# Kernel optimization log

Measured on AMD Instinct MI355X. Metric: run time of the kernel, lower is better.

Reference implementation:

```python
import jax, jax.numpy as jnp
import numpy as np

N = 100000      # nodes
E = 1600000     # edges (avg degree 16)
F_IN = 128      # node feature dim
F_E = 8         # edge feature dim
H = 4           # attention heads (layer 1)
C = 16          # hidden per head
T = 1           # target size (layer 2, heads=1, concat=False)
NEG_SLOPE = 0.2


def setup_inputs() -> dict:
    key = jax.random.key(0)
    ks = jax.random.split(key, 20)
    g = lambda k, shape, fan: (jax.random.normal(k, shape, jnp.float32) / np.sqrt(fan))
    return {
        "x": jax.random.normal(ks[0], (N, F_IN), jnp.float32),
        "edge_index": jax.random.randint(ks[1], (2, E), 0, N, dtype=jnp.int32),
        "edge_attr": jax.random.normal(ks[2], (E, F_E), jnp.float32),
        # layer 1 (in=F_IN, out=C, heads=H, concat=True, edge_dim=F_E)
        "Wl1": g(ks[3], (F_IN, H * C), F_IN),
        "bl1": jnp.zeros((H * C,), jnp.float32),
        "Wr1": g(ks[4], (F_IN, H * C), F_IN),
        "br1": jnp.zeros((H * C,), jnp.float32),
        "We1": g(ks[5], (F_E, H * C), F_E),
        "att1": g(ks[6], (H, C), C),
        "b1": jnp.zeros((H * C,), jnp.float32),
        # layer 2 (in=H*C, out=T, heads=1, concat=False, edge_dim=F_E)
        "Wl2": g(ks[7], (H * C, T), H * C),
        "bl2": jnp.zeros((T,), jnp.float32),
        "Wr2": g(ks[8], (H * C, T), H * C),
        "br2": jnp.zeros((T,), jnp.float32),
        "We2": g(ks[9], (F_E, T), F_E),
        "att2": g(ks[10], (1, T), T),
        "b2": jnp.zeros((T,), jnp.float32),
    }


def _gatv2(x, src, dst, eattr, Wl, bl, Wr, br, We, att, bias, heads, out_ch, concat, n_nodes):
    # add self loops, self-loop edge_attr = mean of edge_attr (PyG fill_value='mean')
    loop = jnp.arange(n_nodes, dtype=src.dtype)
    src_a = jnp.concatenate([src, loop])
    dst_a = jnp.concatenate([dst, loop])
    ea = jnp.concatenate(
        [eattr, jnp.broadcast_to(eattr.mean(axis=0), (n_nodes, eattr.shape[1]))], axis=0)

    xl = (x @ Wl + bl).reshape(n_nodes, heads, out_ch)   # source transform
    xr = (x @ Wr + br).reshape(n_nodes, heads, out_ch)   # target transform
    ee = (ea @ We).reshape(-1, heads, out_ch)            # edge transform (no bias)

    # GATv2: score = att . LeakyReLU(x_l[src] + x_r[dst] + W_e e)
    s = jax.nn.leaky_relu(xl[src_a] + xr[dst_a] + ee, NEG_SLOPE)  # [Ea,H,C]
    logits = jnp.einsum('ehc,hc->eh', s, att)                      # [Ea,H]

    # segment softmax over destination nodes (every node has a self loop)
    m = jax.ops.segment_max(logits, dst_a, num_segments=n_nodes)   # [N,H]
    p = jnp.exp(logits - m[dst_a])
    denom = jax.ops.segment_sum(p, dst_a, num_segments=n_nodes)
    alpha = p / denom[dst_a]                                        # [Ea,H]

    out = jax.ops.segment_sum(xl[src_a] * alpha[:, :, None], dst_a,
                              num_segments=n_nodes)                 # [N,H,C]
    out = out.reshape(n_nodes, heads * out_ch) if concat else out.mean(axis=1)
    return out + bias


def reference(x, edge_index, edge_attr, Wl1, bl1, Wr1, br1, We1, att1, b1,
              Wl2, bl2, Wr2, br2, We2, att2, b2):
    src, dst = edge_index[0], edge_index[1]
    # dropout layers are identity at eval time (training=False)
    h = _gatv2(x, src, dst, edge_attr, Wl1, bl1, Wr1, br1, We1, att1, b1,
               H, C, True, N)
    h = jax.nn.elu(h)
    out = _gatv2(h, src, dst, edge_attr, Wl2, bl2, Wr2, br2, We2, att2, b2,
                 1, T, False, N)
    return out
```

## Files before the change

kernel.cpp:

```cpp
#include <hip/hip_runtime.h>
#include <hip/hip_fp16.h>
#include <math.h>

#define N_NODES 100000
#define N_EDGES 1600000
#define N_ITEMS (N_EDGES + N_NODES)
#define F_IN 128
#define F_E 8
#define HC 64
#define NHEAD 4
#define NEG 0.2f
#define SCAN_BS 1024
#define SCAN_NB ((N_NODES + SCAN_BS - 1) / SCAN_BS)
#define MS_BLOCKS 1024
#define NEG_BIG (-3.0e38f)

union H2I { __half2 h; int i; };

__global__ void mean_sum_kernel(const float* __restrict__ ea, float* __restrict__ partials,
                                unsigned* __restrict__ deg) {
    __shared__ float sh[4][8];
    int stride = gridDim.x * blockDim.x;
    for (int i = blockIdx.x * blockDim.x + threadIdx.x; i < N_NODES; i += stride)
        deg[i] = 1u;
    float acc[8] = {0.f,0.f,0.f,0.f,0.f,0.f,0.f,0.f};
    for (int r = blockIdx.x * blockDim.x + threadIdx.x; r < N_EDGES; r += stride) {
        const float4* p = (const float4*)(ea + (size_t)r * 8);
        float4 a = p[0], b = p[1];
        acc[0] += a.x; acc[1] += a.y; acc[2] += a.z; acc[3] += a.w;
        acc[4] += b.x; acc[5] += b.y; acc[6] += b.z; acc[7] += b.w;
    }
    int wid  = threadIdx.x >> 6;
    int lane = threadIdx.x & 63;
#pragma unroll
    for (int k = 0; k < 8; k++) {
        float v = acc[k];
        for (int off = 32; off; off >>= 1) v += __shfl_down(v, off);
        if (lane == 0) sh[wid][k] = v;
    }
    __syncthreads();
    if (threadIdx.x < 8) {
        float s = sh[0][threadIdx.x] + sh[1][threadIdx.x] + sh[2][threadIdx.x] + sh[3][threadIdx.x];
        partials[blockIdx.x * 8 + threadIdx.x] = s;
    }
}

__global__ void reduce_sum8(const float* __restrict__ partials, float* __restrict__ sum8) {
    int lane = threadIdx.x;
    int c = lane & 7, g = lane >> 3;
    float s = 0.f;
    for (int b = g; b < MS_BLOCKS; b += 8) s += partials[b * 8 + c];
    s += __shfl_xor(s, 8);
    s += __shfl_xor(s, 16);
    s += __shfl_xor(s, 32);
    if (lane < 8) sum8[lane] = s;
}

__global__ void hist_kernel(const int* __restrict__ dst, unsigned* __restrict__ deg) {
    int e = blockIdx.x * blockDim.x + threadIdx.x;
    if (e < N_EDGES) atomicAdd(&deg[dst[e]], 1u);
}

__global__ void scan1(const unsigned* __restrict__ deg, unsigned* __restrict__ local_inc,
                      unsigned* __restrict__ bsum) {
    __shared__ unsigned tmp[SCAN_BS];
    int i = blockIdx.x * SCAN_BS + threadIdx.x;
    unsigned v = (i < N_NODES) ? deg[i] : 0u;
    tmp[threadIdx.x] = v;
    __syncthreads();
    for (int off = 1; off < SCAN_BS; off <<= 1) {
        unsigned add = (threadIdx.x >= (unsigned)off) ? tmp[threadIdx.x - off] : 0u;
        __syncthreads();
        tmp[threadIdx.x] += add;
        __syncthreads();
    }
    if (i < N_NODES) local_inc[i] = tmp[threadIdx.x];
    if (threadIdx.x == SCAN_BS - 1) bsum[blockIdx.x] = tmp[threadIdx.x];
}

__global__ void scan2(unsigned* __restrict__ bsum) {
    __shared__ unsigned tmp[128];
    int t = threadIdx.x;
    unsigned v = (t < SCAN_NB) ? bsum[t] : 0u;
    tmp[t] = v;
    __syncthreads();
    for (int off = 1; off < 128; off <<= 1) {
        unsigned add = (t >= off) ? tmp[t - off] : 0u;
        __syncthreads();
        tmp[t] += add;
        __syncthreads();
    }
    if (t < SCAN_NB) bsum[t] = tmp[t] - v;
}

__global__ void scan3(const unsigned* __restrict__ local_inc, const unsigned* __restrict__ deg,
                      const unsigned* __restrict__ bsum,
                      unsigned* __restrict__ row_start, unsigned* __restrict__ next) {
    int i = blockIdx.x * blockDim.x + threadIdx.x;
    if (i >= N_NODES) return;
    unsigned v = local_inc[i] - deg[i] + bsum[i / SCAN_BS];
    row_start[i] = v;
    next[i] = v;
}

__global__ void scatter_kernel(const int* __restrict__ src, const int* __restrict__ dst,
                               const float* __restrict__ ea, const float* __restrict__ sum8,
                               const float* __restrict__ We2,
                               unsigned* __restrict__ next,
                               int* __restrict__ sorted_src, __half* __restrict__ seah,
                               float* __restrict__ see2) {
    int item = blockIdx.x * blockDim.x + threadIdx.x;
    if (item >= N_ITEMS) return;
    int s, d;
    float4 a, b;
    if (item < N_EDGES) {
        s = src[item]; d = dst[item];
        const float4* p = (const float4*)(ea + (size_t)item * 8);
        a = p[0]; b = p[1];
    } else {
        s = d = item - N_EDGES;
        const float inv = 1.0f / N_EDGES;
        a = make_float4(sum8[0]*inv, sum8[1]*inv, sum8[2]*inv, sum8[3]*inv);
        b = make_float4(sum8[4]*inv, sum8[5]*inv, sum8[6]*inv, sum8[7]*inv);
    }
    float ee2 = a.x*We2[0] + a.y*We2[1] + a.z*We2[2] + a.w*We2[3]
              + b.x*We2[4] + b.y*We2[5] + b.z*We2[6] + b.w*We2[7];
    unsigned pos = atomicAdd(&next[d], 1u);
    sorted_src[pos] = s;
    see2[pos] = ee2;
    H2I p0, p1, p2, p3;
    p0.h = __floats2half2_rn(a.x, a.y);
    p1.h = __floats2half2_rn(a.z, a.w);
    p2.h = __floats2half2_rn(b.x, b.y);
    p3.h = __floats2half2_rn(b.z, b.w);
    *(int4*)(seah + (size_t)pos * 8) = make_int4(p0.i, p1.i, p2.i, p3.i);
}

__global__ __launch_bounds__(256) void gemm1_kernel(
        const float* __restrict__ x,
        const float* __restrict__ Wl, const float* __restrict__ bl,
        const float* __restrict__ Wr, const float* __restrict__ br,
        __half* __restrict__ xlh, float* __restrict__ xr) {
    __shared__ float xs_t[F_IN][36];
    int t = threadIdx.x & 31;
    int g = threadIdx.x >> 5;
    const float* Wsel = (t < 16) ? Wl : Wr;
    const float* bsel = (t < 16) ? bl : br;
    int jc = (t < 16) ? 4 * t : 4 * t - HC;
    float4 bias = *(const float4*)(bsel + jc);

    int n0 = blockIdx.x * 32;
    int row = threadIdx.x >> 3;
    int cq  = threadIdx.x & 7;
#pragma unroll
    for (int r = 0; r < 4; r++) {
        int c = cq * 4 + r * 32;
        float4 v = *(const float4*)(x + (size_t)(n0 + row) * F_IN + c);
        xs_t[c + 0][row] = v.x;
        xs_t[c + 1][row] = v.y;
        xs_t[c + 2][row] = v.z;
        xs_t[c + 3][row] = v.w;
    }
    __syncthreads();
    int nb = g * 4;
    float4 a0 = bias, a1 = bias, a2 = bias, a3 = bias;
#pragma unroll 4
    for (int k = 0; k < F_IN; k++) {
        float4 w  = *(const float4*)(Wsel + k * HC + jc);
        float4 xv = *(const float4*)&xs_t[k][nb];
        a0.x += w.x * xv.x; a0.y += w.y * xv.x; a0.z += w.z * xv.x; a0.w += w.w * xv.x;
        a1.x += w.x * xv.y; a1.y += w.y * xv.y; a1.z += w.z * xv.y; a1.w += w.w * xv.y;
        a2.x += w.x * xv.z; a2.y += w.y * xv.z; a2.z += w.z * xv.z; a2.w += w.w * xv.z;
        a3.x += w.x * xv.w; a3.y += w.y * xv.w; a3.z += w.z * xv.w; a3.w += w.w * xv.w;
    }
    if (t < 16) {
        float4 arr[4] = {a0, a1, a2, a3};
#pragma unroll
        for (int r = 0; r < 4; r++) {
            H2I u0, u1;
            u0.h = __floats2half2_rn(arr[r].x, arr[r].y);
            u1.h = __floats2half2_rn(arr[r].z, arr[r].w);
            *(int2*)(xlh + (size_t)(n0 + nb + r) * HC + jc) = make_int2(u0.i, u1.i);
        }
    } else {
        *(float4*)(xr + (size_t)(n0 + nb + 0) * HC + jc) = a0;
        *(float4*)(xr + (size_t)(n0 + nb + 1) * HC + jc) = a1;
        *(float4*)(xr + (size_t)(n0 + nb + 2) * HC + jc) = a2;
        *(float4*)(xr + (size_t)(n0 + nb + 3) * HC + jc) = a3;
    }
}

__device__ __forceinline__ void load_edge(const int* __restrict__ ssrc,
                                          const __half* __restrict__ seah,
                                          const __half* __restrict__ xlh,
                                          unsigned start, unsigned cnt, unsigned idx, int cl,
                                          bool& valid, float4& e0, float4& e1, float4& xv) {
    valid = (idx < cnt);
    unsigned sf = valid ? start + idx : start;
    int s = ssrc[sf];
    int4 r = *(const int4*)(seah + (size_t)sf * 8);
    H2I h0, h1, h2, h3;
    h0.i = r.x; h1.i = r.y; h2.i = r.z; h3.i = r.w;
    float2 f0 = __half22float2(h0.h), f1 = __half22float2(h1.h);
    float2 f2 = __half22float2(h2.h), f3 = __half22float2(h3.h);
    e0 = make_float4(f0.x, f0.y, f1.x, f1.y);
    e1 = make_float4(f2.x, f2.y, f3.x, f3.y);
    int2 xw = *(const int2*)(xlh + (size_t)s * HC + 4 * cl);
    H2I u0, u1; u0.i = xw.x; u1.i = xw.y;
    float2 g0 = __half22float2(u0.h), g1 = __half22float2(u1.h);
    xv = make_float4(g0.x, g0.y, g1.x, g1.y);
}

__device__ __forceinline__ void edge_update(const float4* __restrict__ we,
                                            const float4& attv, const float4& xrv,
                                            bool valid, const float4& ea0, const float4& ea1,
                                            const float4& xlv,
                                            float& m, float& den, float4& acc) {
    float4 v;
    v.x = xlv.x + xrv.x + ea0.x*we[0].x + ea0.y*we[1].x + ea0.z*we[2].x + ea0.w*we[3].x
                        + ea1.x*we[4].x + ea1.y*we[5].x + ea1.z*we[6].x + ea1.w*we[7].x;
    v.y = xlv.y + xrv.y + ea0.x*we[0].y + ea0.y*we[1].y + ea0.z*we[2].y + ea0.w*we[3].y
                        + ea1.x*we[4].y + ea1.y*we[5].y + ea1.z*we[6].y + ea1.w*we[7].y;
    v.z = xlv.z + xrv.z + ea0.x*we[0].z + ea0.y*we[1].z + ea0.z*we[2].z + ea0.w*we[3].z
                        + ea1.x*we[4].z + ea1.y*we[5].z + ea1.z*we[6].z + ea1.w*we[7].z;
    v.w = xlv.w + xrv.w + ea0.x*we[0].w + ea0.y*we[1].w + ea0.z*we[2].w + ea0.w*we[3].w
                        + ea1.x*we[4].w + ea1.y*we[5].w + ea1.z*we[6].w + ea1.w*we[7].w;
    v.x = v.x > 0.f ? v.x : NEG * v.x;
    v.y = v.y > 0.f ? v.y : NEG * v.y;
    v.z = v.z > 0.f ? v.z : NEG * v.z;
    v.w = v.w > 0.f ? v.w : NEG * v.w;
    float prod = v.x*attv.x + v.y*attv.y + v.z*attv.z + v.w*attv.w;
    prod += __shfl_xor(prod, 1);
    prod += __shfl_xor(prod, 2);
    float logit = valid ? prod : NEG_BIG;
    float mnew  = fmaxf(m, logit);
    float scale = __expf(m - mnew);
    float p     = valid ? __expf(logit - mnew) : 0.f;
    den   = den   * scale + p;
    acc.x = acc.x * scale + p * xlv.x;
    acc.y = acc.y * scale + p * xlv.y;
    acc.z = acc.z * scale + p * xlv.z;
    acc.w = acc.w * scale + p * xlv.w;
    m = mnew;
}

__global__ void gat1_kernel(const unsigned* __restrict__ row_start, const unsigned* __restrict__ deg,
                            const int* __restrict__ ssrc, const __half* __restrict__ seah,
                            const float* __restrict__ We1, const float* __restrict__ att1,
                            const float* __restrict__ b1,
                            const __half* __restrict__ xlh, const float* __restrict__ xr,
                            const float* __restrict__ Wl2, const float* __restrict__ bl2,
                            const float* __restrict__ Wr2, const float* __restrict__ br2,
                            float* __restrict__ xl2, float* __restrict__ xr2) {
    int node = blockIdx.x * (blockDim.x >> 6) + (threadIdx.x >> 6);
    int lane = threadIdx.x & 63;
    if (node >= N_NODES) return;
    int g  = lane >> 4;
    int cl = lane & 15;
    unsigned start = row_start[node];
    unsigned cnt   = deg[node];

    float4 we[8];
#pragma unroll
    for (int k = 0; k < 8; k++) we[k] = *(const float4*)(We1 + k * HC + 4 * cl);
    float4 attv = *(const float4*)(att1 + 4 * cl);
    float4 xrv  = *(const float4*)(xr + (size_t)node * HC + 4 * cl);

    float mA = NEG_BIG, denA = 0.f, mB = NEG_BIG, denB = 0.f;
    float4 accA = make_float4(0.f,0.f,0.f,0.f), accB = make_float4(0.f,0.f,0.f,0.f);

    bool vA_n, vB_n;
    float4 e0A_n, e1A_n, xA_n, e0B_n, e1B_n, xB_n;
    load_edge(ssrc, seah, xlh, start, cnt, g,     cl, vA_n, e0A_n, e1A_n, xA_n);
    load_edge(ssrc, seah, xlh, start, cnt, 4 + g, cl, vB_n, e0B_n, e1B_n, xB_n);

    for (unsigned j = 0; j < cnt; j += 8) {
        bool vA = vA_n, vB = vB_n;
        float4 e0A = e0A_n, e1A = e1A_n, xA = xA_n;
        float4 e0B = e0B_n, e1B = e1B_n, xB = xB_n;
        unsigned jn = j + 8;
        if (jn < cnt) {
            load_edge(ssrc, seah, xlh, start, cnt, jn + g,     cl, vA_n, e0A_n, e1A_n, xA_n);
            load_edge(ssrc, seah, xlh, start, cnt, jn + 4 + g, cl, vB_n, e0B_n, e1B_n, xB_n);
        }
        edge_update(we, attv, xrv, vA, e0A, e1A, xA, mA, denA, accA);
        edge_update(we, attv, xrv, vB, e0B, e1B, xB, mB, denB, accB);
    }
    float m = fmaxf(mA, mB);
    float sA = __expf(mA - m), sB = __expf(mB - m);
    float den = denA * sA + denB * sB;
    float4 acc;
    acc.x = accA.x * sA + accB.x * sB;
    acc.y = accA.y * sA + accB.y * sB;
    acc.z = accA.z * sA + accB.z * sB;
    acc.w = accA.w * sA + accB.w * sB;

    float M = m;
    M = fmaxf(M, __shfl_xor(M, 16));
    M = fmaxf(M, __shfl_xor(M, 32));
    float gs = __expf(m - M);
    den *= gs; acc.x *= gs; acc.y *= gs; acc.z *= gs; acc.w *= gs;
    den   += __shfl_xor(den, 16);   den   += __shfl_xor(den, 32);
    acc.x += __shfl_xor(acc.x, 16); acc.x += __shfl_xor(acc.x, 32);
    acc.y += __shfl_xor(acc.y, 16); acc.y += __shfl_xor(acc.y, 32);
    acc.z += __shfl_xor(acc.z, 16); acc.z += __shfl_xor(acc.z, 32);
    acc.w += __shfl_xor(acc.w, 16); acc.w += __shfl_xor(acc.w, 32);

    float4 b1v  = *(const float4*)(b1 + 4 * cl);
    float4 wl2v = *(const float4*)(Wl2 + 4 * cl);
    float4 wr2v = *(const float4*)(Wr2 + 4 * cl);
    float inv_den = 1.f / den;
    float4 o;
    o.x = acc.x * inv_den + b1v.x;
    o.y = acc.y * inv_den + b1v.y;
    o.z = acc.z * inv_den + b1v.z;
    o.w = acc.w * inv_den + b1v.w;
    o.x = o.x > 0.f ? o.x : expm1f(o.x);
    o.y = o.y > 0.f ? o.y : expm1f(o.y);
    o.z = o.z > 0.f ? o.z : expm1f(o.z);
    o.w = o.w > 0.f ? o.w : expm1f(o.w);
    float sl = o.x*wl2v.x + o.y*wl2v.y + o.z*wl2v.z + o.w*wl2v.w;
    float sr = o.x*wr2v.x + o.y*wr2v.y + o.z*wr2v.z + o.w*wr2v.w;
#pragma unroll
    for (int off = 1; off <= 8; off <<= 1) {
        sl += __shfl_xor(sl, off);
        sr += __shfl_xor(sr, off);
    }
    if (lane == 0) {
        xl2[node] = sl + bl2[0];
        xr2[node] = sr + br2[0];
    }
}

__global__ void gat2_kernel(const unsigned* __restrict__ row_start, const unsigned* __restrict__ deg,
                            const int* __restrict__ sorted_src, const float* __restrict__ see2,
                            const float* __restrict__ att2,
                            const float* __restrict__ xl2, const float* __restrict__ xr2,
                            const float* __restrict__ b2, float* __restrict__ out) {
    int node = blockIdx.x * (blockDim.x >> 6) + (threadIdx.x >> 6);
    int lane = threadIdx.x & 63;
    if (node >= N_NODES) return;
    unsigned start = row_start[node];
    unsigned cnt   = deg[node];
    float xrv = xr2[node];
    float a2  = att2[0];
    float m = -INFINITY, den = 0.f, num = 0.f;
    for (unsigned base = 0; base < cnt; base += 64) {
        unsigned idx = base + lane;
        float logit = -INFINITY, xv = 0.f;
        if (idx < cnt) {
            int s = sorted_src[start + idx];
            float ee = see2[start + idx];
            xv = xl2[s];
            float v = xv + xrv + ee;
            v = v > 0.f ? v : NEG * v;
            logit = a2 * v;
        }
        float mm = logit;
        for (int off = 1; off < 64; off <<= 1) mm = fmaxf(mm, __shfl_xor(mm, off));
        float mnew = fmaxf(m, mm);
        float p  = (idx < cnt) ? __expf(logit - mnew) : 0.f;
        float pn = p * xv;
        for (int off = 1; off < 64; off <<= 1) {
            p  += __shfl_xor(p, off);
            pn += __shfl_xor(pn, off);
        }
        float scale = __expf(m - mnew);
        den = den * scale + p;
        num = num * scale + pn;
        m = mnew;
    }
    if (lane == 0) out[node] = num / den + b2[0];
}

extern "C" void kernel_launch(void* const* d_in, const int* in_sizes, int n_in,
                              void* d_out, int out_size, void* d_ws, size_t ws_size,
                              hipStream_t stream) {
    const float* x    = (const float*)d_in[0];
    const int*   ei   = (const int*)d_in[1];
    const float* ea   = (const float*)d_in[2];
    const float* Wl1  = (const float*)d_in[3];
    const float* bl1  = (const float*)d_in[4];
    const float* Wr1  = (const float*)d_in[5];
    const float* br1  = (const float*)d_in[6];
    const float* We1  = (const float*)d_in[7];
    const float* att1 = (const float*)d_in[8];
    const float* b1   = (const float*)d_in[9];
    const float* Wl2  = (const float*)d_in[10];
    const float* bl2  = (const float*)d_in[11];
    const float* Wr2  = (const float*)d_in[12];
    const float* br2  = (const float*)d_in[13];
    const float* We2  = (const float*)d_in[14];
    const float* att2 = (const float*)d_in[15];
    const float* b2   = (const float*)d_in[16];

    const int* src = ei;
    const int* dst = ei + N_EDGES;

    float* W = (float*)d_ws;
    size_t o = 0;
    float*    sum8      = W + o;               o += 8;
    float*    partials  = W + o;               o += MS_BLOCKS * 8;
    unsigned* deg       = (unsigned*)(W + o);  o += N_NODES;
    unsigned* local_inc = (unsigned*)(W + o);  o += N_NODES;
    unsigned* bsum      = (unsigned*)(W + o);  o += 128;
    unsigned* row_start = (unsigned*)(W + o);  o += N_NODES;
    unsigned* next      = (unsigned*)(W + o);  o += N_NODES;
    int*      ssrc      = (int*)(W + o);       o += N_ITEMS;
    float*    see2      = W + o;               o += N_ITEMS;
    o = (o + 3) & ~(size_t)3;
    __half*   seah      = (__half*)(W + o);    o += (size_t)N_ITEMS * 4;
    __half*   xl1h      = (__half*)(W + o);    o += (size_t)N_NODES * (HC / 2);
    float*    xr1       = W + o;               o += (size_t)N_NODES * HC;
    float*    xl2       = W + o;               o += N_NODES;
    float*    xr2       = W + o;               o += N_NODES;

    mean_sum_kernel<<<MS_BLOCKS, 256, 0, stream>>>(ea, partials, deg);
    reduce_sum8<<<1, 64, 0, stream>>>(partials, sum8);
    hist_kernel<<<(N_EDGES + 255) / 256, 256, 0, stream>>>(dst, deg);
    scan1<<<SCAN_NB, SCAN_BS, 0, stream>>>(deg, local_inc, bsum);
    scan2<<<1, 128, 0, stream>>>(bsum);
    scan3<<<(N_NODES + 255) / 256, 256, 0, stream>>>(local_inc, deg, bsum, row_start, next);
    scatter_kernel<<<(N_ITEMS + 255) / 256, 256, 0, stream>>>(
        src, dst, ea, sum8, We2, next, ssrc, seah, see2);
    gemm1_kernel<<<N_NODES / 32, 256, 0, stream>>>(x, Wl1, bl1, Wr1, br1, xl1h, xr1);
    gat1_kernel<<<(N_NODES + 3) / 4, 256, 0, stream>>>(
        row_start, deg, ssrc, seah, We1, att1, b1, xl1h, xr1,
        Wl2, bl2, Wr2, br2, xl2, xr2);
    gat2_kernel<<<(N_NODES + 3) / 4, 256, 0, stream>>>(
        row_start, deg, ssrc, see2, att2, xl2, xr2, b2, (float*)d_out);
}
```

Baseline: 439.5 us.

## Deepen gather prefetch in gat1 and use shuffle-based block scan

The layer-1 aggregation loop now keeps two stages of edge loads in flight, using raw half-precision registers and double buffering, instead of one. Source indices for the first 64 edges are loaded once per wave and passed around with shuffles, which removes a dependent global load before each feature gather. The scan1 kernel replaces its shared-memory Hillis-Steele loop with a wave-level shuffle scan plus a small cross-wave pass. The deeper prefetch raises register pressure and may lower occupancy.

```diff
diff --git a/kernel.cpp b/kernel.cpp
--- a/kernel.cpp
+++ b/kernel.cpp
@@ -63,19 +63,33 @@
 
 __global__ void scan1(const unsigned* __restrict__ deg, unsigned* __restrict__ local_inc,
                       unsigned* __restrict__ bsum) {
-    __shared__ unsigned tmp[SCAN_BS];
+    __shared__ unsigned wsum[16];
     int i = blockIdx.x * SCAN_BS + threadIdx.x;
+    int lane = threadIdx.x & 63;
+    int wid  = threadIdx.x >> 6;
     unsigned v = (i < N_NODES) ? deg[i] : 0u;
-    tmp[threadIdx.x] = v;
+    unsigned sc = v;
+#pragma unroll
+    for (int off = 1; off < 64; off <<= 1) {
+        unsigned t = __shfl_up(sc, off);
+        if (lane >= off) sc += t;
+    }
+    if (lane == 63) wsum[wid] = sc;
     __syncthreads();
-    for (int off = 1; off < SCAN_BS; off <<= 1) {
-        unsigned add = (threadIdx.x >= (unsigned)off) ? tmp[threadIdx.x - off] : 0u;
-        __syncthreads();
-        tmp[threadIdx.x] += add;
-        __syncthreads();
-    }
-    if (i < N_NODES) local_inc[i] = tmp[threadIdx.x];
-    if (threadIdx.x == SCAN_BS - 1) bsum[blockIdx.x] = tmp[threadIdx.x];
+    if (threadIdx.x < 16) {
+        unsigned w = wsum[threadIdx.x];
+#pragma unroll
+        for (int off = 1; off < 16; off <<= 1) {
+            unsigned t = __shfl_up(w, off);
+            if ((int)threadIdx.x >= off) w += t;
+        }
+        wsum[threadIdx.x] = w;
+    }
+    __syncthreads();
+    unsigned base = wid ? wsum[wid - 1] : 0u;
+    sc += base;
+    if (i < N_NODES) local_inc[i] = sc;
+    if (threadIdx.x == SCAN_BS - 1) bsum[blockIdx.x] = sc;
 }
 
 __global__ void scan2(unsigned* __restrict__ bsum) {
@@ -190,25 +204,20 @@
     }
 }
 
-__device__ __forceinline__ void load_edge(const int* __restrict__ ssrc,
-                                          const __half* __restrict__ seah,
-                                          const __half* __restrict__ xlh,
-                                          unsigned start, unsigned cnt, unsigned idx, int cl,
-                                          bool& valid, float4& e0, float4& e1, float4& xv) {
-    valid = (idx < cnt);
-    unsigned sf = valid ? start + idx : start;
-    int s = ssrc[sf];
-    int4 r = *(const int4*)(seah + (size_t)sf * 8);
-    H2I h0, h1, h2, h3;
-    h0.i = r.x; h1.i = r.y; h2.i = r.z; h3.i = r.w;
+__device__ __forceinline__ float4 sea_lo(const int4& r) {
+    H2I h0, h1; h0.i = r.x; h1.i = r.y;
     float2 f0 = __half22float2(h0.h), f1 = __half22float2(h1.h);
+    return make_float4(f0.x, f0.y, f1.x, f1.y);
+}
+__device__ __forceinline__ float4 sea_hi(const int4& r) {
+    H2I h2, h3; h2.i = r.z; h3.i = r.w;
     float2 f2 = __half22float2(h2.h), f3 = __half22float2(h3.h);
-    e0 = make_float4(f0.x, f0.y, f1.x, f1.y);
-    e1 = make_float4(f2.x, f2.y, f3.x, f3.y);
-    int2 xw = *(const int2*)(xlh + (size_t)s * HC + 4 * cl);
-    H2I u0, u1; u0.i = xw.x; u1.i = xw.y;
+    return make_float4(f2.x, f2.y, f3.x, f3.y);
+}
+__device__ __forceinline__ float4 xl_f(const int2& w) {
+    H2I u0, u1; u0.i = w.x; u1.i = w.y;
     float2 g0 = __half22float2(u0.h), g1 = __half22float2(u1.h);
-    xv = make_float4(g0.x, g0.y, g1.x, g1.y);
+    return make_float4(g0.x, g0.y, g1.x, g1.y);
 }
 
 __device__ __forceinline__ void edge_update(const float4* __restrict__ we,
@@ -260,6 +269,8 @@
     unsigned start = row_start[node];
     unsigned cnt   = deg[node];
 
+    int s_reg = ssrc[start + min((unsigned)lane, cnt - 1)];
+
     float4 we[8];
 #pragma unroll
     for (int k = 0; k < 8; k++) we[k] = *(const float4*)(We1 + k * HC + 4 * cl);
@@ -269,23 +280,40 @@
     float mA = NEG_BIG, denA = 0.f, mB = NEG_BIG, denB = 0.f;
     float4 accA = make_float4(0.f,0.f,0.f,0.f), accB = make_float4(0.f,0.f,0.f,0.f);
 
-    bool vA_n, vB_n;
-    float4 e0A_n, e1A_n, xA_n, e0B_n, e1B_n, xB_n;
-    load_edge(ssrc, seah, xlh, start, cnt, g,     cl, vA_n, e0A_n, e1A_n, xA_n);
-    load_edge(ssrc, seah, xlh, start, cnt, 4 + g, cl, vB_n, e0B_n, e1B_n, xB_n);
-
-    for (unsigned j = 0; j < cnt; j += 8) {
-        bool vA = vA_n, vB = vB_n;
-        float4 e0A = e0A_n, e1A = e1A_n, xA = xA_n;
-        float4 e0B = e0B_n, e1B = e1B_n, xB = xB_n;
-        unsigned jn = j + 8;
-        if (jn < cnt) {
-            load_edge(ssrc, seah, xlh, start, cnt, jn + g,     cl, vA_n, e0A_n, e1A_n, xA_n);
-            load_edge(ssrc, seah, xlh, start, cnt, jn + 4 + g, cl, vB_n, e0B_n, e1B_n, xB_n);
-        }
-        edge_update(we, attv, xrv, vA, e0A, e1A, xA, mA, denA, accA);
-        edge_update(we, attv, xrv, vB, e0B, e1B, xB, mB, denB, accB);
-    }
+    int4 spA0, spA1, spB0, spB1;
+    int2 xpA0, xpA1, xpB0, xpB1;
+
+#define ISSUE(S, JJ) do {                                                      \
+    unsigned iA_ = min((JJ) + (unsigned)g, cnt - 1);                           \
+    unsigned iB_ = min((JJ) + 4u + (unsigned)g, cnt - 1);                      \
+    int sA_ = (iA_ < 64u) ? __shfl(s_reg, (int)iA_) : ssrc[start + iA_];       \
+    int sB_ = (iB_ < 64u) ? __shfl(s_reg, (int)iB_) : ssrc[start + iB_];       \
+    spA##S = *(const int4*)(seah + (size_t)(start + iA_) * 8);                 \
+    xpA##S = *(const int2*)(xlh + (size_t)sA_ * HC + 4 * cl);                  \
+    spB##S = *(const int4*)(seah + (size_t)(start + iB_) * 8);                 \
+    xpB##S = *(const int2*)(xlh + (size_t)sB_ * HC + 4 * cl);                  \
+} while (0)
+
+    ISSUE(0, 0u);
+    ISSUE(1, 8u);
+    for (unsigned j = 0; j < cnt; j += 16) {
+        {
+            float4 e0A = sea_lo(spA0), e1A = sea_hi(spA0), xA = xl_f(xpA0);
+            float4 e0B = sea_lo(spB0), e1B = sea_hi(spB0), xB = xl_f(xpB0);
+            if (j + 16 < cnt) ISSUE(0, j + 16);
+            edge_update(we, attv, xrv, (j + g) < cnt,      e0A, e1A, xA, mA, denA, accA);
+            edge_update(we, attv, xrv, (j + 4 + g) < cnt,  e0B, e1B, xB, mB, denB, accB);
+        }
+        if (j + 8 < cnt) {
+            float4 e0A = sea_lo(spA1), e1A = sea_hi(spA1), xA = xl_f(xpA1);
+            float4 e0B = sea_lo(spB1), e1B = sea_hi(spB1), xB = xl_f(xpB1);
+            if (j + 24 < cnt) ISSUE(1, j + 24);
+            edge_update(we, attv, xrv, (j + 8 + g) < cnt,  e0A, e1A, xA, mA, denA, accA);
+            edge_update(we, attv, xrv, (j + 12 + g) < cnt, e0B, e1B, xB, mB, denB, accB);
+        }
+    }
+#undef ISSUE
+
     float m = fmaxf(mA, mB);
     float sA = __expf(mA - m), sB = __expf(mB - m);
     float den = denA * sA + denB * sB;
```

New measurement: 439.2 us. No clear change (-0.1%).
